# Kernel tuning notes

Measured on AMD Instinct MI355X. Metric: run time of the kernel, lower is better.

## Reference

```python
import jax, jax.numpy as jnp
import numpy as np

N, G, HID, LAT, E_RAND = 20000, 3000, 256, 32, 320000
EPS = 1e-8
NEG_SLOPE = 0.2  # PyG GATv2Conv default leaky_relu slope


def _segment_softmax(logits, seg, n):
    # numerically stable softmax over edges grouped by destination node
    m = jax.ops.segment_max(logits, seg, num_segments=n)
    ex = jnp.exp(logits - m[seg])
    s = jax.ops.segment_sum(ex, seg, num_segments=n)
    return ex / (s[seg] + 1e-16)


def _gatv2(x, src, dst, Wl, Wr, att, b, n):
    # GATv2 (heads=1): score = att . leaky_relu(Wl x_j + Wr x_i)
    xl = x @ Wl  # [N, C] source transform (also the message)
    xr = x @ Wr  # [N, C] destination transform
    e = jax.nn.leaky_relu(xl[src] + xr[dst], NEG_SLOPE)  # [E, C]
    logit = e @ att  # [E]
    alpha = _segment_softmax(logit, dst, n)
    out = jax.ops.segment_sum(alpha[:, None] * xl[src], dst, num_segments=n)
    return out + b


def _log_zinb(x, mu, theta, pi):
    theta = theta[None, :]
    softplus_pi = jax.nn.softplus(-pi)
    log_theta_eps = jnp.log(theta + EPS)
    log_theta_mu_eps = jnp.log(theta + mu + EPS)
    pi_theta_log = -pi + theta * (log_theta_eps - log_theta_mu_eps)
    case_zero = jax.nn.softplus(pi_theta_log) - softplus_pi
    case_nz = (-softplus_pi + pi_theta_log
               + x * (jnp.log(mu + EPS) - log_theta_mu_eps)
               + jax.lax.lgamma(x + theta) - jax.lax.lgamma(theta)
               - jax.lax.lgamma(x + 1.0))
    return jnp.where(x < EPS, case_zero, 0.0) + jnp.where(x > EPS, case_nz, 0.0)


def setup_inputs():
    key = jax.random.key(0)
    ks = jax.random.split(key, 14)
    x = jax.random.randint(ks[0], (N, G), 0, 20).astype(jnp.float32)
    er = jax.random.randint(ks[1], (2, E_RAND), 0, N, dtype=jnp.int32)
    loops = jnp.tile(jnp.arange(N, dtype=jnp.int32)[None, :], (2, 1))
    edge_index = jnp.concatenate([er, loops], axis=1)  # [2, 340000] incl self-loops
    noise = jax.random.normal(ks[2], (N, LAT), dtype=jnp.float32)

    def init(k, shape, fan_in):
        return jax.random.normal(k, shape, dtype=jnp.float32) / np.float32(np.sqrt(fan_in))

    Wl1 = init(ks[3], (G, HID), G); Wr1 = init(ks[4], (G, HID), G)
    att1 = init(ks[5], (HID,), HID); b1 = jnp.zeros((HID,), jnp.float32)
    Wl2 = init(ks[6], (HID, 2 * LAT), HID); Wr2 = init(ks[7], (HID, 2 * LAT), HID)
    att2 = init(ks[8], (2 * LAT,), 2 * LAT); b2 = jnp.zeros((2 * LAT,), jnp.float32)
    Wd1 = init(ks[9], (LAT, HID), LAT); bd1 = jnp.zeros((HID,), jnp.float32)
    Wd2 = init(ks[10], (HID, G), HID); bd2 = jnp.zeros((G,), jnp.float32)
    Wdo = init(ks[11], (HID, G), HID); bdo = jnp.zeros((G,), jnp.float32)
    theta = jax.random.uniform(ks[12], (G,), minval=0.5, maxval=2.0, dtype=jnp.float32)
    return dict(x=x, edge_index=edge_index, noise=noise,
                Wl1=Wl1, Wr1=Wr1, att1=att1, b1=b1,
                Wl2=Wl2, Wr2=Wr2, att2=att2, b2=b2,
                Wd1=Wd1, bd1=bd1, Wd2=Wd2, bd2=bd2, Wdo=Wdo, bdo=bdo,
                theta=theta)


def reference(x, edge_index, noise, Wl1, Wr1, att1, b1, Wl2, Wr2, att2, b2,
              Wd1, bd1, Wd2, bd2, Wdo, bdo, theta):
    n = x.shape[0]
    src, dst = edge_index[0], edge_index[1]
    # --- GATv2 encoder ---
    h = _gatv2(x, src, dst, Wl1, Wr1, att1, b1, n)
    h2 = _gatv2(jax.nn.relu(h), src, dst, Wl2, Wr2, att2, b2, n)  # [N, 2*LAT]
    mu_z, logvar = h2[:, :LAT], h2[:, LAT:]
    # --- reparameterize: std = sqrt(exp(logvar)) ---
    z = mu_z + noise * jnp.exp(0.5 * logvar)
    # --- ZINB decoder ---
    hd = z @ Wd1 + bd1
    mean = jax.nn.softplus(hd @ Wd2 + bd2)
    pi = hd @ Wdo + bdo
    # --- loss: -E[log ZINB] + KL(q(z|x) || N(0,I)) ---
    recon = -jnp.mean(jnp.sum(_log_zinb(x, mean, theta, pi), axis=1))
    kl = jnp.mean(0.5 * jnp.sum(mu_z ** 2 + jnp.exp(logvar) - logvar - 1.0, axis=1))
    return recon + kl
```

## Files before the change

kernel.cpp:

```cpp
#include <hip/hip_runtime.h>
#include <math.h>

#define NN   20000
#define GG   3000
#define HIDD 256
#define LATT 32
#define FEPS 1e-8f

typedef __attribute__((ext_vector_type(8))) __bf16 bf16x8;
typedef __attribute__((ext_vector_type(4))) float f32x4;

__device__ __forceinline__ float fsp(float v) {
    float t = __expf(-fabsf(v));
    return fmaxf(v, 0.f) + __logf(1.f + t);
}
__device__ __forceinline__ float sp_approx(float t) {
    float a = fabsf(t);
    float den = fmaf(a, fmaf(a, fmaf(a, 0.8382f, -1.4958f), 1.87f), 1.f);
    return fmaxf(t, 0.f) + 0.6931472f * __builtin_amdgcn_rcpf(den);
}
__device__ __forceinline__ float lrelu(float v) {
    return v > 0.f ? v : 0.2f * v;
}
__device__ __forceinline__ ushort f2bf(float f) {
    uint b = __float_as_uint(f);
    return (ushort)((b + 0x7FFFu + ((b >> 16) & 1u)) >> 16);
}
__device__ __forceinline__ uint pk2(float a, float b) {
    return (uint)f2bf(a) | ((uint)f2bf(b) << 16);
}
__device__ __forceinline__ void gload16(const void* g, void* l) {
    __builtin_amdgcn_global_load_lds((const __attribute__((address_space(1))) void*)g,
                                     (__attribute__((address_space(3))) void*)l, 16, 0, 0);
}

__global__ void zinb_table(const float* __restrict__ theta, float* __restrict__ tabL,
                           float* __restrict__ logte, int G_) {
    int idx = blockIdx.x * blockDim.x + threadIdx.x;
    if (idx >= G_ * 20) return;
    int g = idx / 20, c = idx % 20;
    float th = theta[g];
    tabL[idx] = lgammaf((float)c + th) - lgammaf(th) - lgammaf((float)c + 1.f);
    if (c == 0) logte[g] = logf(th + FEPS);
}

__global__ void edge_hist(const int* __restrict__ ei, int* __restrict__ cnt, int E) {
    int e = blockIdx.x * blockDim.x + threadIdx.x;
    if (e < E) atomicAdd(&cnt[ei[E + e]], 1);
}

__global__ __launch_bounds__(1024)
void scan_deg(int* __restrict__ cnt_cur, int* __restrict__ rowptr, int Nn) {
    __shared__ int ts[1024];
    int t = threadIdx.x;
    int chunk = (Nn + 1023) / 1024;
    int beg = t * chunk, end = min(beg + chunk, Nn);
    int s = 0;
    for (int i = beg; i < end; i++) s += cnt_cur[i];
    ts[t] = s;
    __syncthreads();
    for (int off = 1; off < 1024; off <<= 1) {
        int v = (t >= off) ? ts[t - off] : 0;
        __syncthreads();
        ts[t] += v;
        __syncthreads();
    }
    int run = (t == 0) ? 0 : ts[t - 1];
    for (int i = beg; i < end; i++) {
        int c = cnt_cur[i];
        rowptr[i] = run;
        cnt_cur[i] = run;
        run += c;
    }
    if (t == 1023) rowptr[Nn] = ts[1023];
}

__global__ void edge_scatter(const int* __restrict__ ei, int* __restrict__ cur,
                             int* __restrict__ eidx, int E) {
    int e = blockIdx.x * blockDim.x + threadIdx.x;
    if (e < E) {
        int p = atomicAdd(&cur[ei[E + e]], 1);
        eidx[p] = e;
    }
}

__global__ __launch_bounds__(256)
void transp_bf16(const float* __restrict__ in, ushort* __restrict__ out,
                 int K, int N, int Kpad) {
    __shared__ ushort t[32][33];
    int k0 = blockIdx.x * 32, n0 = blockIdx.y * 32;
    int tx = threadIdx.x & 31, ty = threadIdx.x >> 5;
    #pragma unroll
    for (int u = 0; u < 32; u += 8) {
        int k = k0 + ty + u, n = n0 + tx;
        t[ty + u][tx] = (k < K && n < N) ? f2bf(in[(size_t)k * N + n]) : (ushort)0;
    }
    __syncthreads();
    #pragma unroll
    for (int u = 0; u < 32; u += 8) {
        int n = n0 + ty + u, k = k0 + tx;
        if (n < N && k < Kpad) out[(size_t)n * Kpad + k] = t[tx][ty + u];
    }
}

__global__ __launch_bounds__(256)
void wcomb(const float* __restrict__ Wd1, const float* __restrict__ bd1,
           const float* __restrict__ Wd2, const float* __restrict__ bd2,
           const float* __restrict__ Wdo, const float* __restrict__ bdo,
           ushort* __restrict__ W2t, ushort* __restrict__ Wot,
           float* __restrict__ b2c, float* __restrict__ boc, int G_) {
    __shared__ float w1s[32 * 256];
    int tid = threadIdx.x;
    for (int i = tid; i < 32 * 256; i += 256) w1s[i] = Wd1[i];
    __syncthreads();
    int gl = tid & 63, rg = tid >> 6;
    int g = blockIdx.x * 64 + gl;
    int gc = min(g, G_ - 1);
    float a2[8], ao[8];
    #pragma unroll
    for (int i = 0; i < 8; i++) { a2[i] = 0.f; ao[i] = 0.f; }
    float ab2 = 0.f, abo = 0.f;
    for (int j = 0; j < 256; j++) {
        float w2 = Wd2[(size_t)j * G_ + gc];
        float wo = Wdo[(size_t)j * G_ + gc];
        if (rg == 0) {
            float b1 = bd1[j];
            ab2 = fmaf(b1, w2, ab2);
            abo = fmaf(b1, wo, abo);
        }
        #pragma unroll
        for (int i = 0; i < 8; i++) {
            float w1 = w1s[(rg * 8 + i) * 256 + j];
            a2[i] = fmaf(w1, w2, a2[i]);
            ao[i] = fmaf(w1, wo, ao[i]);
        }
    }
    if (g < G_) {
        #pragma unroll
        for (int i = 0; i < 8; i++) {
            W2t[(size_t)g * 32 + rg * 8 + i] = f2bf(a2[i]);
            Wot[(size_t)g * 32 + rg * 8 + i] = f2bf(ao[i]);
        }
        if (rg == 0) { b2c[g] = ab2 + bd2[g]; boc[g] = abo + bdo[g]; }
    }
}

__global__ __launch_bounds__(256, 4)
void dec_zinb(const ushort* __restrict__ zb, const ushort* __restrict__ W2t,
              const ushort* __restrict__ Wot, const float* __restrict__ xg,
              const float* __restrict__ tabL, const float* __restrict__ theta,
              const float* __restrict__ logte, const float* __restrict__ b2c,
              const float* __restrict__ boc, double* __restrict__ partsR,
              int M, int G_) {
    __shared__ float tabs[64 * 20];
    __shared__ float thetas[64], thltes[64], bd2s[64], bdos[64];
    __shared__ double redd[4];
    const int tid = threadIdx.x;
    const int nwg = gridDim.x * gridDim.y;
    const int orig = blockIdx.y * gridDim.x + blockIdx.x;
    const int q = nwg >> 3, r = nwg & 7, xcd = orig & 7;
    const int vv = (xcd < r ? xcd * (q + 1) : r * (q + 1) + (xcd - r) * q) + (orig >> 3);
    const int bx = vv % gridDim.x, by = vv / gridDim.x;
    const int m0 = by * 128, n0 = bx * 64;
    const int lane = tid & 63, wid = tid >> 6;
    const int wr = wid >> 1, wc = wid & 1;
    const int frow = lane & 15;
    const int ksl = (lane >> 4) << 3;

    for (int i = tid; i < 64; i += 256) {
        int g = n0 + i;
        bool ok = g < G_;
        float th = ok ? theta[g] : 1.f;
        thetas[i] = th;
        thltes[i] = ok ? th * logte[g] : 0.f;
        bd2s[i]   = ok ? b2c[g] : 0.f;
        bdos[i]   = ok ? boc[g] : 0.f;
    }
    for (int i = tid; i < 64 * 20; i += 256) {
        int g = n0 + i / 20;
        tabs[i] = (g < G_) ? tabL[(size_t)g * 20 + i % 20] : 0.f;
    }

    f32x4 acc1[4][2], acc2[4][2];
    #pragma unroll
    for (int i = 0; i < 4; i++)
        #pragma unroll
        for (int j = 0; j < 2; j++) {
            acc1[i][j] = (f32x4){0.f, 0.f, 0.f, 0.f};
            acc2[i][j] = (f32x4){0.f, 0.f, 0.f, 0.f};
        }

    bf16x8 af[4];
    #pragma unroll
    for (int mi = 0; mi < 4; mi++) {
        int gm = min(m0 + (wr << 6) + (mi << 4) + frow, M - 1);
        af[mi] = *(const bf16x8*)(zb + (size_t)gm * 32 + ksl);
    }
    #pragma unroll
    for (int ni = 0; ni < 2; ni++) {
        int gn = min(n0 + (wc << 5) + (ni << 4) + frow, G_ - 1);
        bf16x8 bf1 = *(const bf16x8*)(W2t + (size_t)gn * 32 + ksl);
        bf16x8 bf2 = *(const bf16x8*)(Wot + (size_t)gn * 32 + ksl);
        #pragma unroll
        for (int mi = 0; mi < 4; mi++) {
            acc1[mi][ni] = __builtin_amdgcn_mfma_f32_16x16x32_bf16(af[mi], bf1, acc1[mi][ni], 0, 0, 0);
            acc2[mi][ni] = __builtin_amdgcn_mfma_f32_16x16x32_bf16(af[mi], bf2, acc2[mi][ni], 0, 0, 0);
        }
    }
    __syncthreads();

    const int lr = (lane >> 4) << 2;
    float lsum = 0.f;
    #pragma unroll
    for (int mi = 0; mi < 4; mi++)
        #pragma unroll
        for (int ni = 0; ni < 2; ni++) {
            int lcol = (wc << 5) + (ni << 4) + frow;
            int gn = n0 + lcol;
            int gmb = m0 + (wr << 6) + (mi << 4) + lr;
            if (gn >= G_) continue;
            float xv4[4];
            #pragma unroll
            for (int j = 0; j < 4; j++) {
                int gm = min(gmb + j, M - 1);
                xv4[j] = xg[(size_t)gm * G_ + gn];
            }
            f32x4 am = acc1[mi][ni], ap = acc2[mi][ni];
            float th = thetas[lcol], thlte = thltes[lcol];
            float bm = bd2s[lcol], bp = bdos[lcol];
            #pragma unroll
            for (int j = 0; j < 4; j++) {
                if (gmb + j >= M) continue;
                float mu  = fsp(am[j] + bm);
                float pi  = ap[j] + bp;
                float spp = fsp(pi);
                float ltme = __logf(th + mu + FEPS);
                float lmu  = __logf(mu + FEPS);
                float xv = xv4[j];
                int xi = (int)(xv + 0.5f);
                float ptl = fmaf(-th, ltme, thlte) - pi;
                float corr = (xv < FEPS) ? sp_approx(-ptl) : 0.f;
                lsum += thlte + tabs[lcol * 20 + xi] - spp
                      - (th + xv) * ltme + xv * lmu + corr;
            }
        }
    #pragma unroll
    for (int off = 32; off; off >>= 1) lsum += __shfl_down(lsum, off);
    if (lane == 0) redd[wid] = (double)lsum;
    __syncthreads();
    if (tid == 0)
        partsR[by * gridDim.x + bx] = redd[0] + redd[1] + redd[2] + redd[3];
}

template<bool ABF>
__global__ __launch_bounds__(512, 4)
void gemm_big(const void* __restrict__ Ap, const ushort* __restrict__ B1t,
              const ushort* __restrict__ B2t, float* __restrict__ C1,
              float* __restrict__ C2, int M, int Kreal, int Kpad, int Nc) {
    __shared__ __align__(16) char lds[49152];
    char* ldsA  = lds;
    char* ldsB1 = lds + 16384;
    char* ldsB2 = lds + 32768;

    const int tid = threadIdx.x;
    const int nwg = gridDim.x * gridDim.y;
    const int orig = blockIdx.y * gridDim.x + blockIdx.x;
    const int q = nwg >> 3, r = nwg & 7, xcd = orig & 7;
    const int vv = (xcd < r ? xcd * (q + 1) : r * (q + 1) + (xcd - r) * q) + (orig >> 3);
    const int bx = vv % gridDim.x, by = vv / gridDim.x;
    const int m0 = by * 128, n0 = bx * 128;
    const int lane = tid & 63, wid = tid >> 6;
    const int wr = wid >> 2, wc = wid & 3;
    const int frow = lane & 15;
    const int fkb = (lane >> 4) << 4;

    f32x4 acc1[4][2], acc2[4][2];
    #pragma unroll
    for (int i = 0; i < 4; i++)
        #pragma unroll
        for (int j = 0; j < 2; j++) {
            acc1[i][j] = (f32x4){0.f, 0.f, 0.f, 0.f};
            acc2[i][j] = (f32x4){0.f, 0.f, 0.f, 0.f};
        }

    const int row_in = lane >> 3;
    const int sch = (lane & 7) ^ (row_in & 7);
    const int ldso = (lane << 4);

    const int nk = Kpad >> 6;
    for (int t = 0; t < nk; t++) {
        const int k0 = t << 6;
        #pragma unroll
        for (int u = 0; u < 2; u++) {
            int s = (wid << 1) + u;
            int grow = n0 + (s << 3) + row_in;
            if (grow > Nc - 1) grow = Nc - 1;
            size_t go = (size_t)grow * Kpad + k0 + (sch << 3);
            gload16(B1t + go, ldsB1 + (s << 10) + ldso);
            gload16(B2t + go, ldsB2 + (s << 10) + ldso);
        }
        if (ABF) {
            #pragma unroll
            for (int u = 0; u < 2; u++) {
                int s = (wid << 1) + u;
                int grow = m0 + (s << 3) + row_in;
                if (grow > M - 1) grow = M - 1;
                size_t go = (size_t)grow * Kpad + k0 + (sch << 3);
                gload16((const ushort*)Ap + go, ldsA + (s << 10) + ldso);
            }
        } else {
            int arow = tid >> 2;
            int acol = (tid & 3) << 4;
            int gm = m0 + arow;
            uint4 w0 = make_uint4(0u, 0u, 0u, 0u), w1 = w0;
            if (gm < M) {
                const float* af = (const float*)Ap + (size_t)gm * Kreal + k0 + acol;
                if (k0 + 64 <= Kreal) {
                    float4 a = ((const float4*)af)[0];
                    float4 b = ((const float4*)af)[1];
                    float4 c = ((const float4*)af)[2];
                    float4 d = ((const float4*)af)[3];
                    w0.x = pk2(a.x, a.y); w0.y = pk2(a.z, a.w);
                    w0.z = pk2(b.x, b.y); w0.w = pk2(b.z, b.w);
                    w1.x = pk2(c.x, c.y); w1.y = pk2(c.z, c.w);
                    w1.z = pk2(d.x, d.y); w1.w = pk2(d.z, d.w);
                } else {
                    float tmp[16];
                    #pragma unroll
                    for (int jj = 0; jj < 16; jj++) {
                        int gk = k0 + acol + jj;
                        tmp[jj] = (gk < Kreal) ? af[jj] : 0.f;
                    }
                    w0.x = pk2(tmp[0], tmp[1]);  w0.y = pk2(tmp[2], tmp[3]);
                    w0.z = pk2(tmp[4], tmp[5]);  w0.w = pk2(tmp[6], tmp[7]);
                    w1.x = pk2(tmp[8], tmp[9]);  w1.y = pk2(tmp[10], tmp[11]);
                    w1.z = pk2(tmp[12], tmp[13]); w1.w = pk2(tmp[14], tmp[15]);
                }
            }
            int o0 = ((arow << 7) + (acol << 1)) ^ ((arow & 7) << 4);
            int o1 = ((arow << 7) + ((acol + 8) << 1)) ^ ((arow & 7) << 4);
            *(uint4*)(ldsA + o0) = w0;
            *(uint4*)(ldsA + o1) = w1;
        }
        __syncthreads();
        #pragma unroll
        for (int kk = 0; kk < 2; kk++) {
            int kb = (kk << 6) + fkb;
            bf16x8 af[4], b1f[2], b2f[2];
            #pragma unroll
            for (int mi = 0; mi < 4; mi++) {
                int rr = (wr << 6) + (mi << 4) + frow;
                int o = ((rr << 7) + kb) ^ ((rr & 7) << 4);
                af[mi] = *(const bf16x8*)(ldsA + o);
            }
            #pragma unroll
            for (int ni = 0; ni < 2; ni++) {
                int rr = (wc << 5) + (ni << 4) + frow;
                int o = ((rr << 7) + kb) ^ ((rr & 7) << 4);
                b1f[ni] = *(const bf16x8*)(ldsB1 + o);
                b2f[ni] = *(const bf16x8*)(ldsB2 + o);
            }
            #pragma unroll
            for (int mi = 0; mi < 4; mi++)
                #pragma unroll
                for (int ni = 0; ni < 2; ni++) {
                    acc1[mi][ni] = __builtin_amdgcn_mfma_f32_16x16x32_bf16(af[mi], b1f[ni], acc1[mi][ni], 0, 0, 0);
                    acc2[mi][ni] = __builtin_amdgcn_mfma_f32_16x16x32_bf16(af[mi], b2f[ni], acc2[mi][ni], 0, 0, 0);
                }
        }
        __syncthreads();
    }

    const int lr = (lane >> 4) << 2;
    #pragma unroll
    for (int mi = 0; mi < 4; mi++)
        #pragma unroll
        for (int ni = 0; ni < 2; ni++) {
            int gmb = m0 + (wr << 6) + (mi << 4) + lr;
            int gn  = n0 + (wc << 5) + (ni << 4) + frow;
            if (gn >= Nc) continue;
            f32x4 v1 = acc1[mi][ni], v2 = acc2[mi][ni];
            #pragma unroll
            for (int j = 0; j < 4; j++) {
                int gm = gmb + j;
                if (gm < M) {
                    C1[(size_t)gm * Nc + gn] = v1[j];
                    C2[(size_t)gm * Nc + gn] = v2[j];
                }
            }
        }
}

__global__ __launch_bounds__(256, 4)
void mfma_dual(const void* __restrict__ Ap, const ushort* __restrict__ B1t,
               const ushort* __restrict__ B2t, float* __restrict__ C1,
               float* __restrict__ C2, int M, int K, int Nc) {
    __shared__ __align__(16) char lds[24576];
    char* ldsA  = lds;
    char* ldsB1 = lds + 8192;
    char* ldsB2 = lds + 16384;

    const int tid = threadIdx.x;
    const int m0 = blockIdx.y * 64, n0 = blockIdx.x * 64;
    const int lane = tid & 63, wid = tid >> 6;
    const int wr = wid >> 1, wc = wid & 1;
    const int frow = lane & 15;
    const int fkb = (lane >> 4) << 4;

    f32x4 acc1[2][2], acc2[2][2];
    #pragma unroll
    for (int i = 0; i < 2; i++)
        #pragma unroll
        for (int j = 0; j < 2; j++) {
            acc1[i][j] = (f32x4){0.f, 0.f, 0.f, 0.f};
            acc2[i][j] = (f32x4){0.f, 0.f, 0.f, 0.f};
        }

    const int nk = (K + 63) >> 6;
    for (int t = 0; t < nk; t++) {
        const int k0 = t << 6;
        #pragma unroll
        for (int u = 0; u < 2; u++) {
            int c = tid + (u << 8);
            int row = c >> 3, col8 = (c & 7) << 3;
            int gm = m0 + row, gk = k0 + col8;
            uint4 w = make_uint4(0u, 0u, 0u, 0u);
            if (gm < M && gk < K)
                w = *(const uint4*)((const ushort*)Ap + (size_t)gm * K + gk);
            int o = ((row << 7) + (col8 << 1)) ^ ((row & 7) << 4);
            *(uint4*)(ldsA + o) = w;
        }
        #pragma unroll
        for (int u = 0; u < 2; u++) {
            int c = tid + (u << 8);
            int row = c >> 3, col8 = (c & 7) << 3;
            int gn = n0 + row, gk = k0 + col8;
            uint4 w1 = make_uint4(0u, 0u, 0u, 0u), w2 = w1;
            if (gn < Nc && gk < K) {
                size_t o = (size_t)gn * K + gk;
                w1 = *(const uint4*)(B1t + o);
                w2 = *(const uint4*)(B2t + o);
            }
            int o = ((row << 7) + (col8 << 1)) ^ ((row & 7) << 4);
            *(uint4*)(ldsB1 + o) = w1;
            *(uint4*)(ldsB2 + o) = w2;
        }
        __syncthreads();
        #pragma unroll
        for (int kk = 0; kk < 2; kk++) {
            int kb = (kk << 6) + fkb;
            bf16x8 af[2], b1f[2], b2f[2];
            #pragma unroll
            for (int mi = 0; mi < 2; mi++) {
                int rr = (wr << 5) + (mi << 4) + frow;
                int o = ((rr << 7) + kb) ^ ((rr & 7) << 4);
                af[mi] = *(const bf16x8*)(ldsA + o);
            }
            #pragma unroll
            for (int ni = 0; ni < 2; ni++) {
                int rr = (wc << 5) + (ni << 4) + frow;
                int o = ((rr << 7) + kb) ^ ((rr & 7) << 4);
                b1f[ni] = *(const bf16x8*)(ldsB1 + o);
                b2f[ni] = *(const bf16x8*)(ldsB2 + o);
            }
            #pragma unroll
            for (int mi = 0; mi < 2; mi++)
                #pragma unroll
                for (int ni = 0; ni < 2; ni++) {
                    acc1[mi][ni] = __builtin_amdgcn_mfma_f32_16x16x32_bf16(af[mi], b1f[ni], acc1[mi][ni], 0, 0, 0);
                    acc2[mi][ni] = __builtin_amdgcn_mfma_f32_16x16x32_bf16(af[mi], b2f[ni], acc2[mi][ni], 0, 0, 0);
                }
        }
        __syncthreads();
    }

    const int lr = (lane >> 4) << 2;
    #pragma unroll
    for (int mi = 0; mi < 2; mi++)
        #pragma unroll
        for (int ni = 0; ni < 2; ni++) {
            int gmb = m0 + (wr << 5) + (mi << 4) + lr;
            int gn  = n0 + (wc << 5) + (ni << 4) + frow;
            if (gn >= Nc) continue;
            f32x4 v1 = acc1[mi][ni], v2 = acc2[mi][ni];
            #pragma unroll
            for (int j = 0; j < 4; j++) {
                int gm = gmb + j;
                if (gm < M) {
                    C1[(size_t)gm * Nc + gn] = v1[j];
                    C2[(size_t)gm * Nc + gn] = v2[j];
                }
            }
        }
}

template<int DW, int OM>
__global__ __launch_bounds__(256)
void gat_attn(const float* __restrict__ xl, const float* __restrict__ xr,
              const float* __restrict__ att, const int* __restrict__ ei,
              const int* __restrict__ rowptr, const int* __restrict__ eidx,
              const float* __restrict__ bias, void* __restrict__ out,
              int D, int Nn) {
    __shared__ float lbuf[4][64];
    int wid = threadIdx.x >> 6, lane = threadIdx.x & 63;
    int n = blockIdx.x * 4 + wid;
    if (n >= Nn) return;
    int k = lane * DW;
    float xrr[DW], ats[DW], hacc[DW];
    if (DW == 4) {
        float4 a4 = *(const float4*)(att + k);
        float4 r4 = *(const float4*)(xr + (size_t)n * D + k);
        ats[0] = a4.x; ats[1] = a4.y; ats[2] = a4.z; ats[3] = a4.w;
        xrr[0] = r4.x; xrr[1] = r4.y; xrr[2] = r4.z; xrr[3] = r4.w;
    } else {
        ats[0] = att[k];
        xrr[0] = xr[(size_t)n * D + k];
    }
    #pragma unroll
    for (int d = 0; d < DW; d++) hacc[d] = 0.f;
    float m = -3.0e38f, ssum = 0.f;
    int beg = rowptr[n], end = rowptr[n + 1];
    for (int c0 = beg; c0 < end; c0 += 64) {
        int cnt = min(64, end - c0);
        for (int j = 0; j < cnt; j++) {
            int e = eidx[c0 + j];
            const float* xs = xl + (size_t)ei[e] * D + k;
            float p;
            if (DW == 4) {
                float4 v = *(const float4*)xs;
                p = ats[0] * lrelu(v.x + xrr[0]) + ats[1] * lrelu(v.y + xrr[1])
                  + ats[2] * lrelu(v.z + xrr[2]) + ats[3] * lrelu(v.w + xrr[3]);
            } else {
                p = ats[0] * lrelu(xs[0] + xrr[0]);
            }
            #pragma unroll
            for (int o2 = 32; o2; o2 >>= 1) p += __shfl_down(p, o2);
            if (lane == 0) lbuf[wid][j] = p;
        }
        float cm = (lane < cnt) ? lbuf[wid][lane] : -3.0e38f;
        #pragma unroll
        for (int o2 = 32; o2; o2 >>= 1) cm = fmaxf(cm, __shfl_xor(cm, o2));
        float mnew = fmaxf(m, cm);
        float scale = __expf(m - mnew);
        ssum *= scale;
        #pragma unroll
        for (int d = 0; d < DW; d++) hacc[d] *= scale;
        for (int j = 0; j < cnt; j++) {
            int e = eidx[c0 + j];
            float w = __expf(lbuf[wid][j] - mnew);
            ssum += w;
            const float* xs = xl + (size_t)ei[e] * D + k;
            if (DW == 4) {
                float4 v = *(const float4*)xs;
                hacc[0] = fmaf(w, v.x, hacc[0]);
                hacc[1] = fmaf(w, v.y, hacc[1]);
                hacc[2] = fmaf(w, v.z, hacc[2]);
                hacc[3] = fmaf(w, v.w, hacc[3]);
            } else {
                hacc[0] = fmaf(w, xs[0], hacc[0]);
            }
        }
        m = mnew;
    }
    float inv = 1.f / (ssum + 1e-16f);
    if (DW == 4) {
        float4 b = *(const float4*)(bias + k);
        float r0 = fmaf(hacc[0], inv, b.x), r1 = fmaf(hacc[1], inv, b.y);
        float r2 = fmaf(hacc[2], inv, b.z), r3 = fmaf(hacc[3], inv, b.w);
        if (OM == 0) {
            *(float4*)((float*)out + (size_t)n * D + k) = make_float4(r0, r1, r2, r3);
        } else {
            ushort4 o;
            o.x = f2bf(fmaxf(r0, 0.f)); o.y = f2bf(fmaxf(r1, 0.f));
            o.z = f2bf(fmaxf(r2, 0.f)); o.w = f2bf(fmaxf(r3, 0.f));
            *(ushort4*)((ushort*)out + (size_t)n * D + k) = o;
        }
    } else {
        float r0 = fmaf(hacc[0], inv, bias[k]);
        if (OM == 0) ((float*)out)[(size_t)n * D + k] = r0;
        else         ((ushort*)out)[(size_t)n * D + k] = f2bf(fmaxf(r0, 0.f));
    }
}

__global__ __launch_bounds__(256)
void z_kl(const float* __restrict__ h2, const float* __restrict__ noise,
          ushort* __restrict__ z, double* __restrict__ partsK, int Nn) {
    __shared__ double rd[4];
    int gid = blockIdx.x * blockDim.x + threadIdx.x;
    int n = gid >> 5, k = gid & 31;
    float kt = 0.f;
    if (n < Nn) {
        float mu = h2[(size_t)n * 64 + k];
        float lv = h2[(size_t)n * 64 + 32 + k];
        float ev = expf(lv);
        z[(size_t)n * 32 + k] = f2bf(mu + noise[(size_t)n * 32 + k] * expf(0.5f * lv));
        kt = 0.5f * (mu * mu + ev - lv - 1.f);
    }
    #pragma unroll
    for (int off = 32; off; off >>= 1) kt += __shfl_down(kt, off);
    int wid = threadIdx.x >> 6, lane = threadIdx.x & 63;
    if (lane == 0) rd[wid] = (double)kt;
    __syncthreads();
    if (threadIdx.x == 0) partsK[blockIdx.x] = rd[0] + rd[1] + rd[2] + rd[3];
}

__global__ __launch_bounds__(256)
void final_reduce(const double* __restrict__ pR, int nR,
                  const double* __restrict__ pK, int nK,
                  float* __restrict__ out, int Nn) {
    __shared__ double sd[256];
    double s = 0.0;
    for (int i = threadIdx.x; i < nR; i += 256) s -= pR[i];
    for (int i = threadIdx.x; i < nK; i += 256) s += pK[i];
    sd[threadIdx.x] = s;
    __syncthreads();
    for (int o = 128; o; o >>= 1) {
        if (threadIdx.x < o) sd[threadIdx.x] += sd[threadIdx.x + o];
        __syncthreads();
    }
    if (threadIdx.x == 0) out[0] = (float)(sd[0] / (double)Nn);
}

extern "C" void kernel_launch(void* const* d_in, const int* in_sizes, int n_in,
                              void* d_out, int out_size, void* d_ws, size_t ws_size,
                              hipStream_t stream) {
    const int N_ = NN, G_ = GG, HID_ = HIDD;
    const int KP1 = 3008;
    const float* x     = (const float*)d_in[0];
    const int*   ei    = (const int*)d_in[1];
    const float* noise = (const float*)d_in[2];
    const float* Wl1   = (const float*)d_in[3];
    const float* Wr1   = (const float*)d_in[4];
    const float* att1  = (const float*)d_in[5];
    const float* b1    = (const float*)d_in[6];
    const float* Wl2   = (const float*)d_in[7];
    const float* Wr2   = (const float*)d_in[8];
    const float* att2  = (const float*)d_in[9];
    const float* b2    = (const float*)d_in[10];
    const float* Wd1   = (const float*)d_in[11];
    const float* bd1   = (const float*)d_in[12];
    const float* Wd2   = (const float*)d_in[13];
    const float* bd2   = (const float*)d_in[14];
    const float* Wdo   = (const float*)d_in[15];
    const float* bdo   = (const float*)d_in[16];
    const float* theta = (const float*)d_in[17];
    const int E = in_sizes[1] / 2;

    const int MB128 = (N_ + 127) / 128;
    const int DGX   = (G_ + 63) / 64;
    const int nR    = DGX * MB128;
    const int nKb   = (N_ * 32) / 256;

    char* base = (char*)d_ws;
    size_t off = 0;
    auto alloc = [&](size_t bytes) -> char* {
        char* p = base + off;
        off = (off + bytes + 255) & ~(size_t)255;
        return p;
    };
    double* partsR = (double*)alloc((size_t)nR * 8);
    double* partsK = (double*)alloc((size_t)nKb * 8);
    float*  tabL  = (float*)alloc((size_t)G_ * 20 * 4);
    float*  logte = (float*)alloc((size_t)G_ * 4);
    int*    rowptr= (int*)alloc((size_t)(N_ + 1) * 4);
    int*    cur   = (int*)alloc((size_t)N_ * 4);
    int*    eidx  = (int*)alloc((size_t)E * 4);
    ushort* Wl1t  = (ushort*)alloc((size_t)HID_ * KP1 * 2);
    ushort* Wr1t  = (ushort*)alloc((size_t)HID_ * KP1 * 2);
    ushort* Wl2t  = (ushort*)alloc((size_t)64 * HID_ * 2);
    ushort* Wr2t  = (ushort*)alloc((size_t)64 * HID_ * 2);
    ushort* W2t   = (ushort*)alloc((size_t)G_ * 32 * 2);
    ushort* Wot   = (ushort*)alloc((size_t)G_ * 32 * 2);
    float*  b2c   = (float*)alloc((size_t)G_ * 4);
    float*  boc   = (float*)alloc((size_t)G_ * 4);
    float*  xl1   = (float*)alloc((size_t)N_ * HID_ * 4);
    float*  xr1   = (float*)alloc((size_t)N_ * HID_ * 4);
    ushort* h_bf  = (ushort*)alloc((size_t)N_ * HID_ * 2);
    float*  xl2   = (float*)alloc((size_t)N_ * 64 * 4);
    float*  xr2   = (float*)alloc((size_t)N_ * 64 * 4);
    float*  h2    = (float*)alloc((size_t)N_ * 64 * 4);
    ushort* zb    = (ushort*)alloc((size_t)N_ * 32 * 2);

    float*  outf = (float*)d_out;

    hipMemsetAsync(cur, 0, N_ * sizeof(int), stream);

    zinb_table<<<(G_ * 20 + 255) / 256, 256, 0, stream>>>(theta, tabL, logte, G_);
    edge_hist<<<(E + 255) / 256, 256, 0, stream>>>(ei, cur, E);
    scan_deg<<<1, 1024, 0, stream>>>(cur, rowptr, N_);
    edge_scatter<<<(E + 255) / 256, 256, 0, stream>>>(ei, cur, eidx, E);

    transp_bf16<<<dim3(KP1 / 32, (HID_ + 31) / 32), 256, 0, stream>>>(Wl1, Wl1t, G_, HID_, KP1);
    transp_bf16<<<dim3(KP1 / 32, (HID_ + 31) / 32), 256, 0, stream>>>(Wr1, Wr1t, G_, HID_, KP1);
    transp_bf16<<<dim3(HID_ / 32, 2), 256, 0, stream>>>(Wl2, Wl2t, HID_, 64, HID_);
    transp_bf16<<<dim3(HID_ / 32, 2), 256, 0, stream>>>(Wr2, Wr2t, HID_, 64, HID_);

    wcomb<<<(G_ + 63) / 64, 256, 0, stream>>>(
        Wd1, bd1, Wd2, bd2, Wdo, bdo, W2t, Wot, b2c, boc, G_);

    gemm_big<false><<<dim3(HID_ / 128, MB128), 512, 0, stream>>>(
        x, Wl1t, Wr1t, xl1, xr1, N_, G_, KP1, HID_);
    gat_attn<4, 1><<<(N_ + 3) / 4, 256, 0, stream>>>(
        xl1, xr1, att1, ei, rowptr, eidx, b1, h_bf, HID_, N_);

    mfma_dual<<<dim3(1, (N_ + 63) / 64), 256, 0, stream>>>(
        h_bf, Wl2t, Wr2t, xl2, xr2, N_, HID_, 64);
    gat_attn<1, 0><<<(N_ + 3) / 4, 256, 0, stream>>>(
        xl2, xr2, att2, ei, rowptr, eidx, b2, h2, 64, N_);

    z_kl<<<nKb, 256, 0, stream>>>(h2, noise, zb, partsK, N_);

    dec_zinb<<<dim3(DGX, MB128), 256, 0, stream>>>(
        zb, W2t, Wot, x, tabL, theta, logte, b2c, boc, partsR, N_, G_);

    final_reduce<<<1, 256, 0, stream>>>(partsR, nR, partsK, nKb, outf, N_);
}
```

Baseline: 643.5 us.

## Double-buffer big GEMM LDS stages and use single-pass online softmax in GAT

The large x@W GEMM now double-buffers its LDS tiles in 96KB of shared memory. It prefetches the next K-slice of B and the fp32 A rows into registers while the MFMAs consume the current slice, which roughly halves the barriers per iteration. The GAT attention kernel drops its two-pass chunked softmax, which gathered each neighbor row twice. It now does a single-pass online softmax that gathers each neighbor once, at the cost of two exps per edge and a serial dependency. The larger LDS footprint lowers occupancy to one 512-thread block per CU.

```diff
diff --git a/kernel.cpp b/kernel.cpp
--- a/kernel.cpp
+++ b/kernel.cpp
@@ -252,15 +252,11 @@
         partsR[by * gridDim.x + bx] = redd[0] + redd[1] + redd[2] + redd[3];
 }
 
-template<bool ABF>
-__global__ __launch_bounds__(512, 4)
-void gemm_big(const void* __restrict__ Ap, const ushort* __restrict__ B1t,
+__global__ __launch_bounds__(512, 1)
+void gemm_big(const float* __restrict__ Ap, const ushort* __restrict__ B1t,
               const ushort* __restrict__ B2t, float* __restrict__ C1,
               float* __restrict__ C2, int M, int Kreal, int Kpad, int Nc) {
-    __shared__ __align__(16) char lds[49152];
-    char* ldsA  = lds;
-    char* ldsB1 = lds + 16384;
-    char* ldsB2 = lds + 32768;
+    __shared__ __align__(16) char lds[98304];
 
     const int tid = threadIdx.x;
     const int nwg = gridDim.x * gridDim.y;
@@ -274,6 +270,16 @@
     const int frow = lane & 15;
     const int fkb = (lane >> 4) << 4;
 
+    const int row_in = lane >> 3;
+    const int sch = (lane & 7) ^ (row_in & 7);
+    const int ldso = (lane << 4);
+    const int arow = tid >> 2;
+    const int acol = (tid & 3) << 4;
+    const int ao0 = ((arow << 7) + (acol << 1)) ^ ((arow & 7) << 4);
+    const int ao1 = ((arow << 7) + ((acol + 8) << 1)) ^ ((arow & 7) << 4);
+    const int gmA = min(m0 + arow, M - 1);
+    const float* arowp = Ap + (size_t)gmA * Kreal;
+
     f32x4 acc1[4][2], acc2[4][2];
     #pragma unroll
     for (int i = 0; i < 4; i++)
@@ -283,66 +289,67 @@
             acc2[i][j] = (f32x4){0.f, 0.f, 0.f, 0.f};
         }
 
-    const int row_in = lane >> 3;
-    const int sch = (lane & 7) ^ (row_in & 7);
-    const int ldso = (lane << 4);
-
-    const int nk = Kpad >> 6;
-    for (int t = 0; t < nk; t++) {
-        const int k0 = t << 6;
+    auto stageB = [&](int k0, char* dB1, char* dB2) {
         #pragma unroll
         for (int u = 0; u < 2; u++) {
             int s = (wid << 1) + u;
             int grow = n0 + (s << 3) + row_in;
             if (grow > Nc - 1) grow = Nc - 1;
             size_t go = (size_t)grow * Kpad + k0 + (sch << 3);
-            gload16(B1t + go, ldsB1 + (s << 10) + ldso);
-            gload16(B2t + go, ldsB2 + (s << 10) + ldso);
-        }
-        if (ABF) {
-            #pragma unroll
-            for (int u = 0; u < 2; u++) {
-                int s = (wid << 1) + u;
-                int grow = m0 + (s << 3) + row_in;
-                if (grow > M - 1) grow = M - 1;
-                size_t go = (size_t)grow * Kpad + k0 + (sch << 3);
-                gload16((const ushort*)Ap + go, ldsA + (s << 10) + ldso);
-            }
+            gload16(B1t + go, dB1 + (s << 10) + ldso);
+            gload16(B2t + go, dB2 + (s << 10) + ldso);
+        }
+    };
+    auto loadA = [&](int k0, float* av) {
+        if (k0 + 64 <= Kreal) {
+            const float* af = arowp + k0 + acol;
+            float4 a = ((const float4*)af)[0];
+            float4 b = ((const float4*)af)[1];
+            float4 c = ((const float4*)af)[2];
+            float4 d = ((const float4*)af)[3];
+            av[0]=a.x; av[1]=a.y; av[2]=a.z; av[3]=a.w;
+            av[4]=b.x; av[5]=b.y; av[6]=b.z; av[7]=b.w;
+            av[8]=c.x; av[9]=c.y; av[10]=c.z; av[11]=c.w;
+            av[12]=d.x; av[13]=d.y; av[14]=d.z; av[15]=d.w;
         } else {
-            int arow = tid >> 2;
-            int acol = (tid & 3) << 4;
-            int gm = m0 + arow;
-            uint4 w0 = make_uint4(0u, 0u, 0u, 0u), w1 = w0;
-            if (gm < M) {
-                const float* af = (const float*)Ap + (size_t)gm * Kreal + k0 + acol;
-                if (k0 + 64 <= Kreal) {
-                    float4 a = ((const float4*)af)[0];
-                    float4 b = ((const float4*)af)[1];
-                    float4 c = ((const float4*)af)[2];
-                    float4 d = ((const float4*)af)[3];
-                    w0.x = pk2(a.x, a.y); w0.y = pk2(a.z, a.w);
-                    w0.z = pk2(b.x, b.y); w0.w = pk2(b.z, b.w);
-                    w1.x = pk2(c.x, c.y); w1.y = pk2(c.z, c.w);
-                    w1.z = pk2(d.x, d.y); w1.w = pk2(d.z, d.w);
-                } else {
-                    float tmp[16];
-                    #pragma unroll
-                    for (int jj = 0; jj < 16; jj++) {
-                        int gk = k0 + acol + jj;
-                        tmp[jj] = (gk < Kreal) ? af[jj] : 0.f;
-                    }
-                    w0.x = pk2(tmp[0], tmp[1]);  w0.y = pk2(tmp[2], tmp[3]);
-                    w0.z = pk2(tmp[4], tmp[5]);  w0.w = pk2(tmp[6], tmp[7]);
-                    w1.x = pk2(tmp[8], tmp[9]);  w1.y = pk2(tmp[10], tmp[11]);
-                    w1.z = pk2(tmp[12], tmp[13]); w1.w = pk2(tmp[14], tmp[15]);
-                }
-            }
-            int o0 = ((arow << 7) + (acol << 1)) ^ ((arow & 7) << 4);
-            int o1 = ((arow << 7) + ((acol + 8) << 1)) ^ ((arow & 7) << 4);
-            *(uint4*)(ldsA + o0) = w0;
-            *(uint4*)(ldsA + o1) = w1;
-        }
-        __syncthreads();
+            #pragma unroll
+            for (int jj = 0; jj < 16; jj++) {
+                int gk = k0 + acol + jj;
+                av[jj] = (gk < Kreal) ? arowp[gk] : 0.f;
+            }
+        }
+    };
+    auto writeA = [&](const float* av, char* dA) {
+        uint4 w0, w1;
+        w0.x = pk2(av[0], av[1]);   w0.y = pk2(av[2], av[3]);
+        w0.z = pk2(av[4], av[5]);   w0.w = pk2(av[6], av[7]);
+        w1.x = pk2(av[8], av[9]);   w1.y = pk2(av[10], av[11]);
+        w1.z = pk2(av[12], av[13]); w1.w = pk2(av[14], av[15]);
+        *(uint4*)(dA + ao0) = w0;
+        *(uint4*)(dA + ao1) = w1;
+    };
+
+    const int nk = Kpad >> 6;
+    {
+        stageB(0, lds + 16384, lds + 32768);
+        float av[16];
+        loadA(0, av);
+        writeA(av, lds);
+    }
+    __syncthreads();
+
+    for (int t = 0; t < nk; t++) {
+        char* cbuf = lds + ((t & 1) ? 49152 : 0);
+        char* nbuf = lds + ((t & 1) ? 0 : 49152);
+        float av[16];
+        const bool more = (t + 1 < nk);
+        if (more) {
+            stageB((t + 1) << 6, nbuf + 16384, nbuf + 32768);
+            loadA((t + 1) << 6, av);
+        }
+        char* ldsA  = cbuf;
+        char* ldsB1 = cbuf + 16384;
+        char* ldsB2 = cbuf + 32768;
         #pragma unroll
         for (int kk = 0; kk < 2; kk++) {
             int kb = (kk << 6) + fkb;
@@ -368,6 +375,7 @@
                     acc2[mi][ni] = __builtin_amdgcn_mfma_f32_16x16x32_bf16(af[mi], b2f[ni], acc2[mi][ni], 0, 0, 0);
                 }
         }
+        if (more) writeA(av, nbuf);
         __syncthreads();
     }
 
@@ -501,7 +509,6 @@
               const int* __restrict__ rowptr, const int* __restrict__ eidx,
               const float* __restrict__ bias, void* __restrict__ out,
               int D, int Nn) {
-    __shared__ float lbuf[4][64];
     int wid = threadIdx.x >> 6, lane = threadIdx.x & 63;
     int n = blockIdx.x * 4 + wid;
     if (n >= Nn) return;
@@ -520,46 +527,28 @@
     for (int d = 0; d < DW; d++) hacc[d] = 0.f;
     float m = -3.0e38f, ssum = 0.f;
     int beg = rowptr[n], end = rowptr[n + 1];
-    for (int c0 = beg; c0 < end; c0 += 64) {
-        int cnt = min(64, end - c0);
-        for (int j = 0; j < cnt; j++) {
-            int e = eidx[c0 + j];
-            const float* xs = xl + (size_t)ei[e] * D + k;
-            float p;
-            if (DW == 4) {
-                float4 v = *(const float4*)xs;
-                p = ats[0] * lrelu(v.x + xrr[0]) + ats[1] * lrelu(v.y + xrr[1])
-                  + ats[2] * lrelu(v.z + xrr[2]) + ats[3] * lrelu(v.w + xrr[3]);
-            } else {
-                p = ats[0] * lrelu(xs[0] + xrr[0]);
-            }
-            #pragma unroll
-            for (int o2 = 32; o2; o2 >>= 1) p += __shfl_down(p, o2);
-            if (lane == 0) lbuf[wid][j] = p;
-        }
-        float cm = (lane < cnt) ? lbuf[wid][lane] : -3.0e38f;
-        #pragma unroll
-        for (int o2 = 32; o2; o2 >>= 1) cm = fmaxf(cm, __shfl_xor(cm, o2));
-        float mnew = fmaxf(m, cm);
-        float scale = __expf(m - mnew);
-        ssum *= scale;
-        #pragma unroll
-        for (int d = 0; d < DW; d++) hacc[d] *= scale;
-        for (int j = 0; j < cnt; j++) {
-            int e = eidx[c0 + j];
-            float w = __expf(lbuf[wid][j] - mnew);
-            ssum += w;
-            const float* xs = xl + (size_t)ei[e] * D + k;
-            if (DW == 4) {
-                float4 v = *(const float4*)xs;
-                hacc[0] = fmaf(w, v.x, hacc[0]);
-                hacc[1] = fmaf(w, v.y, hacc[1]);
-                hacc[2] = fmaf(w, v.z, hacc[2]);
-                hacc[3] = fmaf(w, v.w, hacc[3]);
-            } else {
-                hacc[0] = fmaf(w, xs[0], hacc[0]);
-            }
-        }
+    for (int j = beg; j < end; j++) {
+        int e = eidx[j];
+        const float* xs = xl + (size_t)ei[e] * D + k;
+        float v[DW];
+        float p;
+        if (DW == 4) {
+            float4 v4 = *(const float4*)xs;
+            v[0] = v4.x; v[1] = v4.y; v[2] = v4.z; v[3] = v4.w;
+            p = ats[0] * lrelu(v[0] + xrr[0]) + ats[1] * lrelu(v[1] + xrr[1])
+              + ats[2] * lrelu(v[2] + xrr[2]) + ats[3] * lrelu(v[3] + xrr[3]);
+        } else {
+            v[0] = xs[0];
+            p = ats[0] * lrelu(v[0] + xrr[0]);
+        }
+        #pragma unroll
+        for (int o2 = 32; o2; o2 >>= 1) p += __shfl_xor(p, o2);
+        float mnew = fmaxf(m, p);
+        float sc = __expf(m - mnew);
+        float w  = __expf(p - mnew);
+        ssum = fmaf(ssum, sc, w);
+        #pragma unroll
+        for (int d = 0; d < DW; d++) hacc[d] = fmaf(hacc[d], sc, w * v[d]);
         m = mnew;
     }
     float inv = 1.f / (ssum + 1e-16f);
@@ -698,7 +687,7 @@
     wcomb<<<(G_ + 63) / 64, 256, 0, stream>>>(
         Wd1, bd1, Wd2, bd2, Wdo, bdo, W2t, Wot, b2c, boc, G_);
 
-    gemm_big<false><<<dim3(HID_ / 128, MB128), 512, 0, stream>>>(
+    gemm_big<<<dim3(HID_ / 128, MB128), 512, 0, stream>>>(
         x, Wl1t, Wr1t, xl1, xr1, N_, G_, KP1, HID_);
     gat_attn<4, 1><<<(N_ + 3) / 4, 256, 0, stream>>>(
         xl1, xr1, att1, ei, rowptr, eidx, b1, h_bf, HID_, N_);
```

Measured after the change: 640.1 us. No clear change (-0.5%).
